# Kernel tuning notes

Measured on AMD Instinct MI355X. Metric: run time of the kernel, lower is better.

The kernel has to match this reference:

```python
import jax, jax.numpy as jnp
import numpy as np

H = 32  # hidden size

def _lstm_layer(x, Wih, Whh, bih, bhh):
    # x: [B, T, in]; Wih: [4H, in]; Whh: [4H, H]; biases: [4H]
    # Precompute input contribution for all timesteps (one big GEMM).
    xg = jnp.einsum('bti,gi->btg', x, Wih) + (bih + bhh)  # [B, T, 4H]
    B = x.shape[0]
    h0 = jnp.zeros((B, H), x.dtype)
    c0 = jnp.zeros((B, H), x.dtype)

    def step(carry, xt):
        h, c = carry
        g = xt + h @ Whh.T                      # [B, 4H]
        i, f, gg, o = jnp.split(g, 4, axis=-1)   # PyTorch gate order: i,f,g,o
        i = jax.nn.sigmoid(i)
        f = jax.nn.sigmoid(f)
        gg = jnp.tanh(gg)
        o = jax.nn.sigmoid(o)
        c = f * c + i * gg
        h = o * jnp.tanh(c)
        return (h, c), h

    (_, _), hs = jax.lax.scan(step, (h0, c0), jnp.swapaxes(xg, 0, 1))  # hs: [T, B, H]
    return jnp.swapaxes(hs, 0, 1)  # [B, T, H]


def setup_inputs() -> dict:
    key = jax.random.key(0)
    ks = jax.random.split(key, 11)
    B, T = 4096, 1024
    s = 1.0 / np.sqrt(H)  # PyTorch LSTM init scale
    f32 = jnp.float32
    return {
        'x':    jax.random.normal(ks[0], (B, T, 1), dtype=f32),
        'Wih0': jax.random.uniform(ks[1], (4 * H, 1), dtype=f32, minval=-s, maxval=s),
        'Whh0': jax.random.uniform(ks[2], (4 * H, H), dtype=f32, minval=-s, maxval=s),
        'bih0': jax.random.uniform(ks[3], (4 * H,), dtype=f32, minval=-s, maxval=s),
        'bhh0': jax.random.uniform(ks[4], (4 * H,), dtype=f32, minval=-s, maxval=s),
        'Wih1': jax.random.uniform(ks[5], (4 * H, H), dtype=f32, minval=-s, maxval=s),
        'Whh1': jax.random.uniform(ks[6], (4 * H, H), dtype=f32, minval=-s, maxval=s),
        'bih1': jax.random.uniform(ks[7], (4 * H,), dtype=f32, minval=-s, maxval=s),
        'bhh1': jax.random.uniform(ks[8], (4 * H,), dtype=f32, minval=-s, maxval=s),
        'Wfc':  jax.random.uniform(ks[9], (1, H), dtype=f32, minval=-s, maxval=s),
        'bfc':  jax.random.uniform(ks[10], (1,), dtype=f32, minval=-s, maxval=s),
    }


def reference(x, Wih0, Whh0, bih0, bhh0, Wih1, Whh1, bih1, bhh1, Wfc, bfc):
    h1 = _lstm_layer(x, Wih0, Whh0, bih0, bhh0)   # [B, T, H]
    h2 = _lstm_layer(h1, Wih1, Whh1, bih1, bhh1)  # [B, T, H]
    last = h2[:, -1, :]                            # [B, H]
    return last @ Wfc.T + bfc                      # [B, 1]
```

## Files before the change

### kernel.cpp

```cpp
#include <hip/hip_runtime.h>

#define HSZ  32
#define TLEN 1024
#define PS   40

typedef _Float16 half8 __attribute__((ext_vector_type(8)));
typedef float    f32x4 __attribute__((ext_vector_type(4)));

__device__ __forceinline__ float rcp_f(float x){ return __builtin_amdgcn_rcpf(x); }
__device__ __forceinline__ float exp2_f(float x){ return __builtin_amdgcn_exp2f(x); }
#define SCL_S (-1.442695040888963f)
#define SCL_T ( 2.885390081777927f)

__device__ __forceinline__ f32x4 mfma16(half8 a, half8 b, f32x4 c){
  return __builtin_amdgcn_mfma_f32_16x16x32_f16(a, b, c, 0, 0, 0);
}
__device__ __forceinline__ void lds_barrier(){
  asm volatile("s_waitcnt lgkmcnt(0)\n\ts_barrier" ::: "memory");
}

#define ACT4(A0,A1,A2,A3, CV, IV, FV, GV, OV)                  \
  { float Zi_ = exp2_f(A0), Zf_ = exp2_f(A1);                  \
    float Zg_ = exp2_f(A2), Zo_ = exp2_f(A3);                  \
    float di_ = 1.f+Zi_, df_ = 1.f+Zf_;                        \
    float dg_ = 1.f+Zg_, dq_ = 1.f+Zo_;                        \
    float r1_ = rcp_f(di_*df_); IV = r1_*df_; FV = r1_*di_;    \
    float r2_ = rcp_f(dg_*dq_);                                \
    GV = fmaf(-2.f, r2_*dq_, 1.f); OV = r2_*dg_;               \
    CV = fmaf(FV, CV, IV*GV); }

#define TANHPAIR(CA, CB, OA, OB, HA, HB)                       \
  { float ZA_ = exp2_f(SCL_T*(CA)), ZB_ = exp2_f(SCL_T*(CB));  \
    float dA_ = 1.f+ZA_, dB_ = 1.f+ZB_;                        \
    float re_ = rcp_f(dA_*dB_);                                \
    float qA_ = re_*dB_*(OA), qB_ = re_*dA_*(OB);              \
    HA = fmaf(-2.f, qA_, OA); HB = fmaf(-2.f, qB_, OB); }

__global__ __launch_bounds__(512, 2) void lstm2_pc(
    const float* __restrict__ x,
    const float* __restrict__ Wih0, const float* __restrict__ Whh0,
    const float* __restrict__ bih0, const float* __restrict__ bhh0,
    const float* __restrict__ Wih1, const float* __restrict__ Whh1,
    const float* __restrict__ bih1, const float* __restrict__ bhh1,
    const float* __restrict__ Wfc,  const float* __restrict__ bfc,
    float* __restrict__ out, int Tn)
{
  __shared__ __align__(16) _Float16 hpl[2][2][16*PS];

  const int tid = threadIdx.x;
  const int w   = tid >> 6;
  const int l   = tid & 63;
  const int col = l & 15;
  const int g   = l >> 4;
  const int wl  = w & 3;
  const int b0  = blockIdx.x * 16;
  const bool isL0 = (w < 4);

  const int rdI = col*PS + 8*g;
  const int wrA = col*PS + 8*wl + g;
  const int wrB = wrA + 4;
  const float sA = ((col & 3) == 2) ? SCL_T : SCL_S;
  const float scj[4] = {SCL_S, SCL_S, SCL_T, SCL_S};
  const f32x4 zero4 = {0.f, 0.f, 0.f, 0.f};

  for (int i = tid; i < 2*2*16*PS; i += 512) (&hpl[0][0][0])[i] = (_Float16)0.0f;

  float wxA[4], wxB[4], bsA[4], bsB[4];
  #pragma unroll
  for (int j = 0; j < 4; ++j){
    int rA = 32*j + 8*wl + g, rB = rA + 4;
    wxA[j] = Wih0[rA] * scj[j];
    wxB[j] = Wih0[rB] * scj[j];
    bsA[j] = (bih0[rA] + bhh0[rA]) * scj[j];
    bsB[j] = (bih1 == bih1 ? (bih0[rB] + bhh0[rB]) : 0.f) * scj[j];
  }
  const float* xp = x + (size_t)(b0 + col) * Tn;

  __syncthreads();

  if (isL0){
    float x0 = xp[0];
    float c0A = 0.f, c0B = 0.f, iA,fA,gA,oA, iB,fB,gB,oB, h0A, h0B;
    ACT4(fmaf(x0,wxA[0],bsA[0]), fmaf(x0,wxA[1],bsA[1]),
         fmaf(x0,wxA[2],bsA[2]), fmaf(x0,wxA[3],bsA[3]), c0A, iA,fA,gA,oA);
    ACT4(fmaf(x0,wxB[0],bsB[0]), fmaf(x0,wxB[1],bsB[1]),
         fmaf(x0,wxB[2],bsB[2]), fmaf(x0,wxB[3],bsB[3]), c0B, iB,fB,gB,oB);
    TANHPAIR(c0A, c0B, oA, oB, h0A, h0B);
    hpl[0][0][wrA] = (_Float16)h0A;
    hpl[0][0][wrB] = (_Float16)h0B;
    wxA[0] = wxA[0];
    ;
  }
  __syncthreads();

  float h1Av = 0.f, h1Bv = 0.f;

  if (isL0){
    const int prowA = 32*(col & 3) + 8*wl + (col >> 2);
    half8 WhA, WlA, WhB, WlB;
    {
      const float* pA = Whh0 + prowA*HSZ + 8*g;
      const float* pB = pA + 4*HSZ;
      #pragma unroll
      for (int j = 0; j < 8; ++j){
        float vA = pA[j]*sA, vB = pB[j]*sA;
        _Float16 a = (_Float16)vA; WhA[j] = a; WlA[j] = (_Float16)(vA - (float)a);
        _Float16 b = (_Float16)vB; WhB[j] = b; WlB[j] = (_Float16)(vB - (float)b);
      }
    }
    float c0A = 0.f, c0B = 0.f;
    {
      float x0 = xp[0];
      float iA,fA,gA,oA, iB,fB,gB,oB;
      ACT4(fmaf(x0,wxA[0],bsA[0]), fmaf(x0,wxA[1],bsA[1]),
           fmaf(x0,wxA[2],bsA[2]), fmaf(x0,wxA[3],bsA[3]), c0A, iA,fA,gA,oA);
      ACT4(fmaf(x0,wxB[0],bsB[0]), fmaf(x0,wxB[1],bsB[1]),
           fmaf(x0,wxB[2],bsB[2]), fmaf(x0,wxB[3],bsB[3]), c0B, iB,fB,gB,oB);
    }
    half8 Bh0 = *(const half8*)&hpl[0][0][rdI];
    float xv = xp[1];

#define L0STEP(Q, XNI)                                                     \
    {                                                                      \
      float xn = xp[(XNI)];                                                \
      f32x4 eA, eB;                                                        \
      eA[0]=fmaf(xv,wxA[0],bsA[0]); eA[1]=fmaf(xv,wxA[1],bsA[1]);          \
      eA[2]=fmaf(xv,wxA[2],bsA[2]); eA[3]=fmaf(xv,wxA[3],bsA[3]);          \
      eB[0]=fmaf(xv,wxB[0],bsB[0]); eB[1]=fmaf(xv,wxB[1],bsB[1]);          \
      eB[2]=fmaf(xv,wxB[2],bsB[2]); eB[3]=fmaf(xv,wxB[3],bsB[3]);          \
      __builtin_amdgcn_s_setprio(1);                                       \
      eA = mfma16(WhA, Bh0, eA);  eB = mfma16(WhB, Bh0, eB);               \
      eA = mfma16(WlA, Bh0, eA);  eB = mfma16(WlB, Bh0, eB);               \
      __builtin_amdgcn_s_setprio(0);                                       \
      float iA,fA,gA,oA, iB,fB,gB,oB, h0A, h0B;                            \
      ACT4(eA[0],eA[1],eA[2],eA[3], c0A, iA,fA,gA,oA);                     \
      ACT4(eB[0],eB[1],eB[2],eB[3], c0B, iB,fB,gB,oB);                     \
      TANHPAIR(c0A, c0B, oA, oB, h0A, h0B);                                \
      hpl[(Q)][0][wrA] = (_Float16)h0A;                                    \
      hpl[(Q)][0][wrB] = (_Float16)h0B;                                    \
      lds_barrier();                                                       \
      Bh0 = *(const half8*)&hpl[(Q)][0][rdI];                              \
      xv = xn;                                                             \
    }

    for (int T0 = 0; T0 < Tn; T0 += 2){
      L0STEP(1, (T0+2 < Tn) ? T0+2 : Tn-1);
      L0STEP(0, (T0+3 < Tn) ? T0+3 : Tn-1);
    }
#undef L0STEP
  } else {
    const int prowA = 32*(col & 3) + 8*wl + (col >> 2);
    half8 WIhA, WIlA, WIhB, WIlB, WHhA, WHlA, WHhB, WHlB;
    {
      const float* iA_ = Wih1 + prowA*HSZ + 8*g;
      const float* iB_ = iA_ + 4*HSZ;
      const float* hA_ = Whh1 + prowA*HSZ + 8*g;
      const float* hB_ = hA_ + 4*HSZ;
      #pragma unroll
      for (int j = 0; j < 8; ++j){
        float v0 = iA_[j]*sA, v1 = iB_[j]*sA, v2 = hA_[j]*sA, v3 = hB_[j]*sA;
        _Float16 a = (_Float16)v0; WIhA[j] = a; WIlA[j] = (_Float16)(v0 - (float)a);
        _Float16 b = (_Float16)v1; WIhB[j] = b; WIlB[j] = (_Float16)(v1 - (float)b);
        _Float16 c = (_Float16)v2; WHhA[j] = c; WHlA[j] = (_Float16)(v2 - (float)c);
        _Float16 d = (_Float16)v3; WHhB[j] = d; WHlB[j] = (_Float16)(v3 - (float)d);
      }
    }
    f32x4 bias1A, bias1B;
    #pragma unroll
    for (int j = 0; j < 4; ++j){
      int rA = 32*j + 8*wl + g, rB = rA + 4;
      bias1A[j] = (bih1[rA] + bhh1[rA]) * scj[j];
      bias1B[j] = (bih1[rB] + bhh1[rB]) * scj[j];
    }
    float c1A = 0.f, c1B = 0.f;
    half8 Bh0 = *(const half8*)&hpl[0][0][rdI];
    half8 Bh1 = *(const half8*)&hpl[0][1][rdI];

#define L1STEP(Q)                                                          \
    {                                                                      \
      f32x4 uA, uB, vvA, vvB;                                              \
      __builtin_amdgcn_s_setprio(1);                                       \
      uA  = mfma16(WHhA, Bh1, bias1A);  uB  = mfma16(WHhB, Bh1, bias1B);   \
      vvA = mfma16(WIhA, Bh0, zero4);   vvB = mfma16(WIhB, Bh0, zero4);    \
      uA  = mfma16(WHlA, Bh1, uA);      uB  = mfma16(WHlB, Bh1, uB);       \
      vvA = mfma16(WIlA, Bh0, vvA);     vvB = mfma16(WIlB, Bh0, vvB);      \
      __builtin_amdgcn_s_setprio(0);                                       \
      f32x4 aA = uA + vvA, aB = uB + vvB;                                  \
      float iA,fA,gA,oA, iB,fB,gB,oB;                                      \
      ACT4(aA[0],aA[1],aA[2],aA[3], c1A, iA,fA,gA,oA);                     \
      ACT4(aB[0],aB[1],aB[2],aB[3], c1B, iB,fB,gB,oB);                     \
      TANHPAIR(c1A, c1B, oA, oB, h1Av, h1Bv);                              \
      hpl[(Q)][1][wrA] = (_Float16)h1Av;                                   \
      hpl[(Q)][1][wrB] = (_Float16)h1Bv;                                   \
      lds_barrier();                                                       \
      Bh0 = *(const half8*)&hpl[(Q)][0][rdI];                              \
      Bh1 = *(const half8*)&hpl[(Q)][1][rdI];                              \
    }

    for (int T0 = 0; T0 < Tn; T0 += 2){
      L1STEP(1);
      L1STEP(0);
    }
#undef L1STEP
  }

  __syncthreads();
  float* sc = (float*)&hpl[0][0][0];
  if (w >= 4){
    sc[(8*wl + g)*17 + col]     = h1Av;
    sc[(8*wl + 4 + g)*17 + col] = h1Bv;
  }
  __syncthreads();
  if (tid < 16){
    float acc = bfc[0];
    #pragma unroll 8
    for (int k = 0; k < HSZ; ++k) acc = fmaf(sc[k*17 + tid], Wfc[k], acc);
    out[b0 + tid] = acc;
  }
}

extern "C" void kernel_launch(void* const* d_in, const int* in_sizes, int n_in,
                              void* d_out, int out_size, void* d_ws, size_t ws_size,
                              hipStream_t stream) {
  const float* x    = (const float*)d_in[0];
  const float* Wih0 = (const float*)d_in[1];
  const float* Whh0 = (const float*)d_in[2];
  const float* bih0 = (const float*)d_in[3];
  const float* bhh0 = (const float*)d_in[4];
  const float* Wih1 = (const float*)d_in[5];
  const float* Whh1 = (const float*)d_in[6];
  const float* bih1 = (const float*)d_in[7];
  const float* bhh1 = (const float*)d_in[8];
  const float* Wfc  = (const float*)d_in[9];
  const float* bfc  = (const float*)d_in[10];
  float* out = (float*)d_out;

  const int Tn = TLEN;
  const int B  = in_sizes[0] / Tn;

  dim3 block(512);
  dim3 grid(B / 16);
  hipLaunchKernelGGL(lstm2_pc, grid, block, 0, stream,
                     x, Wih0, Whh0, bih0, bhh0, Wih1, Whh1, bih1, bhh1,
                     Wfc, bfc, out, Tn);
}
```

Measured before the change: 411.8 us.

## Split LSTM gate work across 16 waves per block instead of 8

The block grows from 8 to 16 waves: 8 waves for layer 0 and 8 for layer 1. Each wave now handles one 16-row slice of the gate matrix instead of two, which halves the MFMA and activation work per wave on the serial per-timestep critical path. The cost is more waves meeting at every per-step barrier and higher occupancy demands, with launch bounds raised to 1024 threads and 4 blocks per CU. Whether the per-step latency actually drops depends on barrier overhead versus the shortened dependency chain.

```diff
diff --git a/kernel.cpp b/kernel.cpp
--- a/kernel.cpp
+++ b/kernel.cpp
@@ -29,14 +29,12 @@
     GV = fmaf(-2.f, r2_*dq_, 1.f); OV = r2_*dg_;               \
     CV = fmaf(FV, CV, IV*GV); }
 
-#define TANHPAIR(CA, CB, OA, OB, HA, HB)                       \
-  { float ZA_ = exp2_f(SCL_T*(CA)), ZB_ = exp2_f(SCL_T*(CB));  \
-    float dA_ = 1.f+ZA_, dB_ = 1.f+ZB_;                        \
-    float re_ = rcp_f(dA_*dB_);                                \
-    float qA_ = re_*dB_*(OA), qB_ = re_*dA_*(OB);              \
-    HA = fmaf(-2.f, qA_, OA); HB = fmaf(-2.f, qB_, OB); }
-
-__global__ __launch_bounds__(512, 2) void lstm2_pc(
+#define HOUT(CV, OV, HV)                                       \
+  { float Zc_ = exp2_f(SCL_T*(CV));                            \
+    float rc_ = rcp_f(1.f + Zc_);                              \
+    HV = fmaf(-2.f, rc_*(OV), OV); }
+
+__global__ __launch_bounds__(1024, 4) void lstm2_w16(
     const float* __restrict__ x,
     const float* __restrict__ Wih0, const float* __restrict__ Whh0,
     const float* __restrict__ bih0, const float* __restrict__ bhh0,
@@ -52,92 +50,89 @@
   const int l   = tid & 63;
   const int col = l & 15;
   const int g   = l >> 4;
-  const int wl  = w & 3;
   const int b0  = blockIdx.x * 16;
-  const bool isL0 = (w < 4);
+  const bool isL0 = (w < 8);
+  const int wl  = isL0 ? w : (w - 8);
+  const int st  = 4*wl + g;
 
   const int rdI = col*PS + 8*g;
-  const int wrA = col*PS + 8*wl + g;
-  const int wrB = wrA + 4;
+  const int wrI = col*PS + st;
   const float sA = ((col & 3) == 2) ? SCL_T : SCL_S;
   const float scj[4] = {SCL_S, SCL_S, SCL_T, SCL_S};
   const f32x4 zero4 = {0.f, 0.f, 0.f, 0.f};
-
-  for (int i = tid; i < 2*2*16*PS; i += 512) (&hpl[0][0][0])[i] = (_Float16)0.0f;
-
-  float wxA[4], wxB[4], bsA[4], bsB[4];
-  #pragma unroll
-  for (int j = 0; j < 4; ++j){
-    int rA = 32*j + 8*wl + g, rB = rA + 4;
-    wxA[j] = Wih0[rA] * scj[j];
-    wxB[j] = Wih0[rB] * scj[j];
-    bsA[j] = (bih0[rA] + bhh0[rA]) * scj[j];
-    bsB[j] = (bih1 == bih1 ? (bih0[rB] + bhh0[rB]) : 0.f) * scj[j];
-  }
+  const int prow = 32*(col & 3) + 4*wl + (col >> 2);
+
+  for (int i = tid; i < 2*2*16*PS; i += 1024) (&hpl[0][0][0])[i] = (_Float16)0.0f;
+
+  half8 WAh, WAl, WBh, WBl;
+  f32x4 bias1;
+  float wx[4], bs0[4];
+  half8 WIh, WIl;
   const float* xp = x + (size_t)(b0 + col) * Tn;
+
+  if (isL0){
+    const float* p0 = Whh0 + prow*HSZ + 8*g;
+    #pragma unroll
+    for (int j = 0; j < 8; ++j){
+      float v0 = p0[j]*sA;
+      _Float16 a = (_Float16)v0; WAh[j] = a; WAl[j] = (_Float16)(v0 - (float)a);
+    }
+    #pragma unroll
+    for (int j = 0; j < 4; ++j){
+      int r  = 32*j + st;
+      wx[j]  = Wih0[r] * scj[j];
+      bs0[j] = (bih0[r] + bhh0[r]) * scj[j];
+    }
+  } else {
+    const float* pH = Whh1 + prow*HSZ + 8*g;
+    const float* pI = Wih1 + prow*HSZ + 8*g;
+    #pragma unroll
+    for (int j = 0; j < 8; ++j){
+      float v2 = pH[j]*sA, v1 = pI[j]*sA;
+      _Float16 c = (_Float16)v2; WAh[j] = c; WAl[j] = (_Float16)(v2 - (float)c);
+      _Float16 b = (_Float16)v1; WIh[j] = b; WIl[j] = (_Float16)(v1 - (float)b);
+    }
+    #pragma unroll
+    for (int j = 0; j < 4; ++j){
+      int r = 32*j + st;
+      bias1[j] = (bih1[r] + bhh1[r]) * scj[j];
+    }
+  }
+  (void)WBh; (void)WBl;
+
+  float cSt = 0.f, hFin = 0.f;
 
   __syncthreads();
 
   if (isL0){
     float x0 = xp[0];
-    float c0A = 0.f, c0B = 0.f, iA,fA,gA,oA, iB,fB,gB,oB, h0A, h0B;
-    ACT4(fmaf(x0,wxA[0],bsA[0]), fmaf(x0,wxA[1],bsA[1]),
-         fmaf(x0,wxA[2],bsA[2]), fmaf(x0,wxA[3],bsA[3]), c0A, iA,fA,gA,oA);
-    ACT4(fmaf(x0,wxB[0],bsB[0]), fmaf(x0,wxB[1],bsB[1]),
-         fmaf(x0,wxB[2],bsB[2]), fmaf(x0,wxB[3],bsB[3]), c0B, iB,fB,gB,oB);
-    TANHPAIR(c0A, c0B, oA, oB, h0A, h0B);
-    hpl[0][0][wrA] = (_Float16)h0A;
-    hpl[0][0][wrB] = (_Float16)h0B;
-    wxA[0] = wxA[0];
-    ;
-  }
-  __syncthreads();
-
-  float h1Av = 0.f, h1Bv = 0.f;
+    float iv, fv, gv, ov;
+    ACT4(fmaf(x0,wx[0],bs0[0]), fmaf(x0,wx[1],bs0[1]),
+         fmaf(x0,wx[2],bs0[2]), fmaf(x0,wx[3],bs0[3]), cSt, iv,fv,gv,ov);
+    float h0;
+    HOUT(cSt, ov, h0);
+    hpl[0][0][wrI] = (_Float16)h0;
+  }
+  __syncthreads();
 
   if (isL0){
-    const int prowA = 32*(col & 3) + 8*wl + (col >> 2);
-    half8 WhA, WlA, WhB, WlB;
-    {
-      const float* pA = Whh0 + prowA*HSZ + 8*g;
-      const float* pB = pA + 4*HSZ;
-      #pragma unroll
-      for (int j = 0; j < 8; ++j){
-        float vA = pA[j]*sA, vB = pB[j]*sA;
-        _Float16 a = (_Float16)vA; WhA[j] = a; WlA[j] = (_Float16)(vA - (float)a);
-        _Float16 b = (_Float16)vB; WhB[j] = b; WlB[j] = (_Float16)(vB - (float)b);
-      }
-    }
-    float c0A = 0.f, c0B = 0.f;
-    {
-      float x0 = xp[0];
-      float iA,fA,gA,oA, iB,fB,gB,oB;
-      ACT4(fmaf(x0,wxA[0],bsA[0]), fmaf(x0,wxA[1],bsA[1]),
-           fmaf(x0,wxA[2],bsA[2]), fmaf(x0,wxA[3],bsA[3]), c0A, iA,fA,gA,oA);
-      ACT4(fmaf(x0,wxB[0],bsB[0]), fmaf(x0,wxB[1],bsB[1]),
-           fmaf(x0,wxB[2],bsB[2]), fmaf(x0,wxB[3],bsB[3]), c0B, iB,fB,gB,oB);
-    }
     half8 Bh0 = *(const half8*)&hpl[0][0][rdI];
     float xv = xp[1];
 
 #define L0STEP(Q, XNI)                                                     \
     {                                                                      \
       float xn = xp[(XNI)];                                                \
-      f32x4 eA, eB;                                                        \
-      eA[0]=fmaf(xv,wxA[0],bsA[0]); eA[1]=fmaf(xv,wxA[1],bsA[1]);          \
-      eA[2]=fmaf(xv,wxA[2],bsA[2]); eA[3]=fmaf(xv,wxA[3],bsA[3]);          \
-      eB[0]=fmaf(xv,wxB[0],bsB[0]); eB[1]=fmaf(xv,wxB[1],bsB[1]);          \
-      eB[2]=fmaf(xv,wxB[2],bsB[2]); eB[3]=fmaf(xv,wxB[3],bsB[3]);          \
+      f32x4 e;                                                             \
+      e[0]=fmaf(xv,wx[0],bs0[0]); e[1]=fmaf(xv,wx[1],bs0[1]);              \
+      e[2]=fmaf(xv,wx[2],bs0[2]); e[3]=fmaf(xv,wx[3],bs0[3]);              \
       __builtin_amdgcn_s_setprio(1);                                       \
-      eA = mfma16(WhA, Bh0, eA);  eB = mfma16(WhB, Bh0, eB);               \
-      eA = mfma16(WlA, Bh0, eA);  eB = mfma16(WlB, Bh0, eB);               \
+      e = mfma16(WAh, Bh0, e);                                             \
+      e = mfma16(WAl, Bh0, e);                                             \
       __builtin_amdgcn_s_setprio(0);                                       \
-      float iA,fA,gA,oA, iB,fB,gB,oB, h0A, h0B;                            \
-      ACT4(eA[0],eA[1],eA[2],eA[3], c0A, iA,fA,gA,oA);                     \
-      ACT4(eB[0],eB[1],eB[2],eB[3], c0B, iB,fB,gB,oB);                     \
-      TANHPAIR(c0A, c0B, oA, oB, h0A, h0B);                                \
-      hpl[(Q)][0][wrA] = (_Float16)h0A;                                    \
-      hpl[(Q)][0][wrB] = (_Float16)h0B;                                    \
+      float iv, fv, gv, ov, h0;                                            \
+      ACT4(e[0],e[1],e[2],e[3], cSt, iv,fv,gv,ov);                         \
+      HOUT(cSt, ov, h0);                                                   \
+      hpl[(Q)][0][wrI] = (_Float16)h0;                                     \
       lds_barrier();                                                       \
       Bh0 = *(const half8*)&hpl[(Q)][0][rdI];                              \
       xv = xn;                                                             \
@@ -149,49 +144,23 @@
     }
 #undef L0STEP
   } else {
-    const int prowA = 32*(col & 3) + 8*wl + (col >> 2);
-    half8 WIhA, WIlA, WIhB, WIlB, WHhA, WHlA, WHhB, WHlB;
-    {
-      const float* iA_ = Wih1 + prowA*HSZ + 8*g;
-      const float* iB_ = iA_ + 4*HSZ;
-      const float* hA_ = Whh1 + prowA*HSZ + 8*g;
-      const float* hB_ = hA_ + 4*HSZ;
-      #pragma unroll
-      for (int j = 0; j < 8; ++j){
-        float v0 = iA_[j]*sA, v1 = iB_[j]*sA, v2 = hA_[j]*sA, v3 = hB_[j]*sA;
-        _Float16 a = (_Float16)v0; WIhA[j] = a; WIlA[j] = (_Float16)(v0 - (float)a);
-        _Float16 b = (_Float16)v1; WIhB[j] = b; WIlB[j] = (_Float16)(v1 - (float)b);
-        _Float16 c = (_Float16)v2; WHhA[j] = c; WHlA[j] = (_Float16)(v2 - (float)c);
-        _Float16 d = (_Float16)v3; WHhB[j] = d; WHlB[j] = (_Float16)(v3 - (float)d);
-      }
-    }
-    f32x4 bias1A, bias1B;
-    #pragma unroll
-    for (int j = 0; j < 4; ++j){
-      int rA = 32*j + 8*wl + g, rB = rA + 4;
-      bias1A[j] = (bih1[rA] + bhh1[rA]) * scj[j];
-      bias1B[j] = (bih1[rB] + bhh1[rB]) * scj[j];
-    }
-    float c1A = 0.f, c1B = 0.f;
     half8 Bh0 = *(const half8*)&hpl[0][0][rdI];
     half8 Bh1 = *(const half8*)&hpl[0][1][rdI];
 
 #define L1STEP(Q)                                                          \
     {                                                                      \
-      f32x4 uA, uB, vvA, vvB;                                              \
+      f32x4 u, vv;                                                         \
       __builtin_amdgcn_s_setprio(1);                                       \
-      uA  = mfma16(WHhA, Bh1, bias1A);  uB  = mfma16(WHhB, Bh1, bias1B);   \
-      vvA = mfma16(WIhA, Bh0, zero4);   vvB = mfma16(WIhB, Bh0, zero4);    \
-      uA  = mfma16(WHlA, Bh1, uA);      uB  = mfma16(WHlB, Bh1, uB);       \
-      vvA = mfma16(WIlA, Bh0, vvA);     vvB = mfma16(WIlB, Bh0, vvB);      \
+      u  = mfma16(WAh, Bh1, bias1);                                        \
+      vv = mfma16(WIh, Bh0, zero4);                                        \
+      u  = mfma16(WAl, Bh1, u);                                            \
+      vv = mfma16(WIl, Bh0, vv);                                           \
       __builtin_amdgcn_s_setprio(0);                                       \
-      f32x4 aA = uA + vvA, aB = uB + vvB;                                  \
-      float iA,fA,gA,oA, iB,fB,gB,oB;                                      \
-      ACT4(aA[0],aA[1],aA[2],aA[3], c1A, iA,fA,gA,oA);                     \
-      ACT4(aB[0],aB[1],aB[2],aB[3], c1B, iB,fB,gB,oB);                     \
-      TANHPAIR(c1A, c1B, oA, oB, h1Av, h1Bv);                              \
-      hpl[(Q)][1][wrA] = (_Float16)h1Av;                                   \
-      hpl[(Q)][1][wrB] = (_Float16)h1Bv;                                   \
+      f32x4 a = u + vv;                                                    \
+      float iv, fv, gv, ov;                                                \
+      ACT4(a[0],a[1],a[2],a[3], cSt, iv,fv,gv,ov);                         \
+      HOUT(cSt, ov, hFin);                                                 \
+      hpl[(Q)][1][wrI] = (_Float16)hFin;                                   \
       lds_barrier();                                                       \
       Bh0 = *(const half8*)&hpl[(Q)][0][rdI];                              \
       Bh1 = *(const half8*)&hpl[(Q)][1][rdI];                              \
@@ -206,9 +175,8 @@
 
   __syncthreads();
   float* sc = (float*)&hpl[0][0][0];
-  if (w >= 4){
-    sc[(8*wl + g)*17 + col]     = h1Av;
-    sc[(8*wl + 4 + g)*17 + col] = h1Bv;
+  if (!isL0){
+    sc[st*17 + col] = hFin;
   }
   __syncthreads();
   if (tid < 16){
@@ -238,9 +206,9 @@
   const int Tn = TLEN;
   const int B  = in_sizes[0] / Tn;
 
-  dim3 block(512);
+  dim3 block(1024);
   dim3 grid(B / 16);
-  hipLaunchKernelGGL(lstm2_pc, grid, block, 0, stream,
+  hipLaunchKernelGGL(lstm2_w16, grid, block, 0, stream,
                      x, Wih0, Whh0, bih0, bhh0, Wih1, Whh1, bih1, bhh1,
                      Wfc, bfc, out, Tn);
 }
```

Result: no change. 408.6 us (-0.8%).

## Skew layer-0 and layer-1 phases with two barriers per step

Applied to the files above, without the earlier changes.

Restructures the per-timestep schedule so layer-0 waves run their MFMA for the next step right after publishing h0, while layer-1 waves do their MFMAs and then their activations in a separate barrier phase. Each step now has two barriers, so layer-0 and layer-1 activation work sit in different phases and overlap with the other layer's matrix work instead of both hitting the same critical path. Layer-1 now keeps a single h1 buffer and reads h0 from a double buffer, and the setprio hints are dropped. The price is an extra barrier per timestep, and the two layers depend on a careful phase alignment for correctness.

```diff
diff --git a/kernel.cpp b/kernel.cpp
--- a/kernel.cpp
+++ b/kernel.cpp
@@ -19,15 +19,16 @@
   asm volatile("s_waitcnt lgkmcnt(0)\n\ts_barrier" ::: "memory");
 }
 
-#define ACT4(A0,A1,A2,A3, CV, IV, FV, GV, OV)                  \
+#define ACT4(A0,A1,A2,A3, CV, OV)                              \
   { float Zi_ = exp2_f(A0), Zf_ = exp2_f(A1);                  \
     float Zg_ = exp2_f(A2), Zo_ = exp2_f(A3);                  \
     float di_ = 1.f+Zi_, df_ = 1.f+Zf_;                        \
     float dg_ = 1.f+Zg_, dq_ = 1.f+Zo_;                        \
-    float r1_ = rcp_f(di_*df_); IV = r1_*df_; FV = r1_*di_;    \
+    float r1_ = rcp_f(di_*df_);                                \
+    float IV_ = r1_*df_, FV_ = r1_*di_;                        \
     float r2_ = rcp_f(dg_*dq_);                                \
-    GV = fmaf(-2.f, r2_*dq_, 1.f); OV = r2_*dg_;               \
-    CV = fmaf(FV, CV, IV*GV); }
+    float GV_ = fmaf(-2.f, r2_*dq_, 1.f); OV = r2_*dg_;        \
+    CV = fmaf(FV_, CV, IV_*GV_); }
 
 #define TANHPAIR(CA, CB, OA, OB, HA, HB)                       \
   { float ZA_ = exp2_f(SCL_T*(CA)), ZB_ = exp2_f(SCL_T*(CB));  \
@@ -36,7 +37,7 @@
     float qA_ = re_*dB_*(OA), qB_ = re_*dA_*(OB);              \
     HA = fmaf(-2.f, qA_, OA); HB = fmaf(-2.f, qB_, OB); }
 
-__global__ __launch_bounds__(512, 2) void lstm2_pc(
+__global__ __launch_bounds__(512, 2) void lstm2_skew(
     const float* __restrict__ x,
     const float* __restrict__ Wih0, const float* __restrict__ Whh0,
     const float* __restrict__ bih0, const float* __restrict__ bhh0,
@@ -45,16 +46,18 @@
     const float* __restrict__ Wfc,  const float* __restrict__ bfc,
     float* __restrict__ out, int Tn)
 {
-  __shared__ __align__(16) _Float16 hpl[2][2][16*PS];
+  __shared__ __align__(16) _Float16 H0[2][16*PS];
+  __shared__ __align__(16) _Float16 H1[16*PS];
+  __shared__ float sc[32*17];
 
   const int tid = threadIdx.x;
   const int w   = tid >> 6;
   const int l   = tid & 63;
   const int col = l & 15;
   const int g   = l >> 4;
-  const int wl  = w & 3;
   const int b0  = blockIdx.x * 16;
   const bool isL0 = (w < 4);
+  const int wl  = isL0 ? w : (w - 4);
 
   const int rdI = col*PS + 8*g;
   const int wrA = col*PS + 8*wl + g;
@@ -62,151 +65,150 @@
   const float sA = ((col & 3) == 2) ? SCL_T : SCL_S;
   const float scj[4] = {SCL_S, SCL_S, SCL_T, SCL_S};
   const f32x4 zero4 = {0.f, 0.f, 0.f, 0.f};
-
-  for (int i = tid; i < 2*2*16*PS; i += 512) (&hpl[0][0][0])[i] = (_Float16)0.0f;
-
+  const int prowA = 32*(col & 3) + 8*wl + (col >> 2);
+
+  for (int i = tid; i < (2*16 + 16)*PS; i += 512) (&H0[0][0])[i] = (_Float16)0.0f;
+
+  const float* xp = x + (size_t)(b0 + col) * Tn;
+  const int Tm1 = Tn - 1;
+
+  half8 WhA, WlA, WhB, WlB;
+  half8 WIhA, WIlA, WIhB, WIlB;
   float wxA[4], wxB[4], bsA[4], bsB[4];
-  #pragma unroll
-  for (int j = 0; j < 4; ++j){
-    int rA = 32*j + 8*wl + g, rB = rA + 4;
-    wxA[j] = Wih0[rA] * scj[j];
-    wxB[j] = Wih0[rB] * scj[j];
-    bsA[j] = (bih0[rA] + bhh0[rA]) * scj[j];
-    bsB[j] = (bih1 == bih1 ? (bih0[rB] + bhh0[rB]) : 0.f) * scj[j];
-  }
-  const float* xp = x + (size_t)(b0 + col) * Tn;
-
-  __syncthreads();
+  f32x4 bias1A, bias1B;
 
   if (isL0){
-    float x0 = xp[0];
-    float c0A = 0.f, c0B = 0.f, iA,fA,gA,oA, iB,fB,gB,oB, h0A, h0B;
-    ACT4(fmaf(x0,wxA[0],bsA[0]), fmaf(x0,wxA[1],bsA[1]),
-         fmaf(x0,wxA[2],bsA[2]), fmaf(x0,wxA[3],bsA[3]), c0A, iA,fA,gA,oA);
-    ACT4(fmaf(x0,wxB[0],bsB[0]), fmaf(x0,wxB[1],bsB[1]),
-         fmaf(x0,wxB[2],bsB[2]), fmaf(x0,wxB[3],bsB[3]), c0B, iB,fB,gB,oB);
-    TANHPAIR(c0A, c0B, oA, oB, h0A, h0B);
-    hpl[0][0][wrA] = (_Float16)h0A;
-    hpl[0][0][wrB] = (_Float16)h0B;
-    wxA[0] = wxA[0];
-    ;
-  }
-  __syncthreads();
-
-  float h1Av = 0.f, h1Bv = 0.f;
-
-  if (isL0){
-    const int prowA = 32*(col & 3) + 8*wl + (col >> 2);
-    half8 WhA, WlA, WhB, WlB;
-    {
-      const float* pA = Whh0 + prowA*HSZ + 8*g;
-      const float* pB = pA + 4*HSZ;
-      #pragma unroll
-      for (int j = 0; j < 8; ++j){
-        float vA = pA[j]*sA, vB = pB[j]*sA;
-        _Float16 a = (_Float16)vA; WhA[j] = a; WlA[j] = (_Float16)(vA - (float)a);
-        _Float16 b = (_Float16)vB; WhB[j] = b; WlB[j] = (_Float16)(vB - (float)b);
-      }
-    }
-    float c0A = 0.f, c0B = 0.f;
-    {
-      float x0 = xp[0];
-      float iA,fA,gA,oA, iB,fB,gB,oB;
-      ACT4(fmaf(x0,wxA[0],bsA[0]), fmaf(x0,wxA[1],bsA[1]),
-           fmaf(x0,wxA[2],bsA[2]), fmaf(x0,wxA[3],bsA[3]), c0A, iA,fA,gA,oA);
-      ACT4(fmaf(x0,wxB[0],bsB[0]), fmaf(x0,wxB[1],bsB[1]),
-           fmaf(x0,wxB[2],bsB[2]), fmaf(x0,wxB[3],bsB[3]), c0B, iB,fB,gB,oB);
-    }
-    half8 Bh0 = *(const half8*)&hpl[0][0][rdI];
-    float xv = xp[1];
-
-#define L0STEP(Q, XNI)                                                     \
-    {                                                                      \
-      float xn = xp[(XNI)];                                                \
-      f32x4 eA, eB;                                                        \
-      eA[0]=fmaf(xv,wxA[0],bsA[0]); eA[1]=fmaf(xv,wxA[1],bsA[1]);          \
-      eA[2]=fmaf(xv,wxA[2],bsA[2]); eA[3]=fmaf(xv,wxA[3],bsA[3]);          \
-      eB[0]=fmaf(xv,wxB[0],bsB[0]); eB[1]=fmaf(xv,wxB[1],bsB[1]);          \
-      eB[2]=fmaf(xv,wxB[2],bsB[2]); eB[3]=fmaf(xv,wxB[3],bsB[3]);          \
-      __builtin_amdgcn_s_setprio(1);                                       \
-      eA = mfma16(WhA, Bh0, eA);  eB = mfma16(WhB, Bh0, eB);               \
-      eA = mfma16(WlA, Bh0, eA);  eB = mfma16(WlB, Bh0, eB);               \
-      __builtin_amdgcn_s_setprio(0);                                       \
-      float iA,fA,gA,oA, iB,fB,gB,oB, h0A, h0B;                            \
-      ACT4(eA[0],eA[1],eA[2],eA[3], c0A, iA,fA,gA,oA);                     \
-      ACT4(eB[0],eB[1],eB[2],eB[3], c0B, iB,fB,gB,oB);                     \
-      TANHPAIR(c0A, c0B, oA, oB, h0A, h0B);                                \
-      hpl[(Q)][0][wrA] = (_Float16)h0A;                                    \
-      hpl[(Q)][0][wrB] = (_Float16)h0B;                                    \
-      lds_barrier();                                                       \
-      Bh0 = *(const half8*)&hpl[(Q)][0][rdI];                              \
-      xv = xn;                                                             \
-    }
-
-    for (int T0 = 0; T0 < Tn; T0 += 2){
-      L0STEP(1, (T0+2 < Tn) ? T0+2 : Tn-1);
-      L0STEP(0, (T0+3 < Tn) ? T0+3 : Tn-1);
-    }
-#undef L0STEP
+    const float* pA = Whh0 + prowA*HSZ + 8*g;
+    const float* pB = pA + 4*HSZ;
+    #pragma unroll
+    for (int j = 0; j < 8; ++j){
+      float vA = pA[j]*sA, vB = pB[j]*sA;
+      _Float16 a = (_Float16)vA; WhA[j] = a; WlA[j] = (_Float16)(vA - (float)a);
+      _Float16 b = (_Float16)vB; WhB[j] = b; WlB[j] = (_Float16)(vB - (float)b);
+    }
+    #pragma unroll
+    for (int j = 0; j < 4; ++j){
+      int rA = 32*j + 8*wl + g, rB = rA + 4;
+      wxA[j] = Wih0[rA] * scj[j];
+      wxB[j] = Wih0[rB] * scj[j];
+      bsA[j] = (bih0[rA] + bhh0[rA]) * scj[j];
+      bsB[j] = (bih0[rB] + bhh0[rB]) * scj[j];
+    }
   } else {
-    const int prowA = 32*(col & 3) + 8*wl + (col >> 2);
-    half8 WIhA, WIlA, WIhB, WIlB, WHhA, WHlA, WHhB, WHlB;
-    {
-      const float* iA_ = Wih1 + prowA*HSZ + 8*g;
-      const float* iB_ = iA_ + 4*HSZ;
-      const float* hA_ = Whh1 + prowA*HSZ + 8*g;
-      const float* hB_ = hA_ + 4*HSZ;
-      #pragma unroll
-      for (int j = 0; j < 8; ++j){
-        float v0 = iA_[j]*sA, v1 = iB_[j]*sA, v2 = hA_[j]*sA, v3 = hB_[j]*sA;
-        _Float16 a = (_Float16)v0; WIhA[j] = a; WIlA[j] = (_Float16)(v0 - (float)a);
-        _Float16 b = (_Float16)v1; WIhB[j] = b; WIlB[j] = (_Float16)(v1 - (float)b);
-        _Float16 c = (_Float16)v2; WHhA[j] = c; WHlA[j] = (_Float16)(v2 - (float)c);
-        _Float16 d = (_Float16)v3; WHhB[j] = d; WHlB[j] = (_Float16)(v3 - (float)d);
-      }
-    }
-    f32x4 bias1A, bias1B;
+    const float* hA_ = Whh1 + prowA*HSZ + 8*g;
+    const float* hB_ = hA_ + 4*HSZ;
+    const float* iA_ = Wih1 + prowA*HSZ + 8*g;
+    const float* iB_ = iA_ + 4*HSZ;
+    #pragma unroll
+    for (int j = 0; j < 8; ++j){
+      float v0 = hA_[j]*sA, v1 = hB_[j]*sA, v2 = iA_[j]*sA, v3 = iB_[j]*sA;
+      _Float16 a = (_Float16)v0; WhA[j]  = a; WlA[j]  = (_Float16)(v0 - (float)a);
+      _Float16 b = (_Float16)v1; WhB[j]  = b; WlB[j]  = (_Float16)(v1 - (float)b);
+      _Float16 c = (_Float16)v2; WIhA[j] = c; WIlA[j] = (_Float16)(v2 - (float)c);
+      _Float16 d = (_Float16)v3; WIhB[j] = d; WIlB[j] = (_Float16)(v3 - (float)d);
+    }
     #pragma unroll
     for (int j = 0; j < 4; ++j){
       int rA = 32*j + 8*wl + g, rB = rA + 4;
       bias1A[j] = (bih1[rA] + bhh1[rA]) * scj[j];
       bias1B[j] = (bih1[rB] + bhh1[rB]) * scj[j];
     }
-    float c1A = 0.f, c1B = 0.f;
-    half8 Bh0 = *(const half8*)&hpl[0][0][rdI];
-    half8 Bh1 = *(const half8*)&hpl[0][1][rdI];
-
-#define L1STEP(Q)                                                          \
+  }
+
+  float c0A = 0.f, c0B = 0.f;
+  float c1A = 0.f, c1B = 0.f;
+  float h1Av = 0.f, h1Bv = 0.f;
+
+  __syncthreads();
+
+  if (isL0){
+    float x0 = xp[0];
+    float oA_, oB_, h0A, h0B;
+    ACT4(fmaf(x0,wxA[0],bsA[0]), fmaf(x0,wxA[1],bsA[1]),
+         fmaf(x0,wxA[2],bsA[2]), fmaf(x0,wxA[3],bsA[3]), c0A, oA_);
+    ACT4(fmaf(x0,wxB[0],bsB[0]), fmaf(x0,wxB[1],bsB[1]),
+         fmaf(x0,wxB[2],bsB[2]), fmaf(x0,wxB[3],bsB[3]), c0B, oB_);
+    TANHPAIR(c0A, c0B, oA_, oB_, h0A, h0B);
+    H0[0][wrA] = (_Float16)h0A;
+    H0[0][wrB] = (_Float16)h0B;
+  }
+  __syncthreads();
+
+  if (isL0){
+    half8 Bh0 = *(const half8*)&H0[0][rdI];
+    f32x4 eA, eB;
+    {
+      float x1 = xp[1];
+      eA[0] = fmaf(x1, wxA[0], bsA[0]); eA[1] = fmaf(x1, wxA[1], bsA[1]);
+      eA[2] = fmaf(x1, wxA[2], bsA[2]); eA[3] = fmaf(x1, wxA[3], bsA[3]);
+      eB[0] = fmaf(x1, wxB[0], bsB[0]); eB[1] = fmaf(x1, wxB[1], bsB[1]);
+      eB[2] = fmaf(x1, wxB[2], bsB[2]); eB[3] = fmaf(x1, wxB[3], bsB[3]);
+      eA = mfma16(WhA, Bh0, eA);  eB = mfma16(WhB, Bh0, eB);
+      eA = mfma16(WlA, Bh0, eA);  eB = mfma16(WlB, Bh0, eB);
+    }
+    float xc = xp[2 <= Tm1 ? 2 : Tm1];
+
+#define L0BODY(Q, XNI)                                                     \
     {                                                                      \
-      f32x4 uA, uB, vvA, vvB;                                              \
-      __builtin_amdgcn_s_setprio(1);                                       \
-      uA  = mfma16(WHhA, Bh1, bias1A);  uB  = mfma16(WHhB, Bh1, bias1B);   \
-      vvA = mfma16(WIhA, Bh0, zero4);   vvB = mfma16(WIhB, Bh0, zero4);    \
-      uA  = mfma16(WHlA, Bh1, uA);      uB  = mfma16(WHlB, Bh1, uB);       \
-      vvA = mfma16(WIlA, Bh0, vvA);     vvB = mfma16(WIlB, Bh0, vvB);      \
-      __builtin_amdgcn_s_setprio(0);                                       \
-      f32x4 aA = uA + vvA, aB = uB + vvB;                                  \
-      float iA,fA,gA,oA, iB,fB,gB,oB;                                      \
-      ACT4(aA[0],aA[1],aA[2],aA[3], c1A, iA,fA,gA,oA);                     \
-      ACT4(aB[0],aB[1],aB[2],aB[3], c1B, iB,fB,gB,oB);                     \
-      TANHPAIR(c1A, c1B, oA, oB, h1Av, h1Bv);                              \
-      hpl[(Q)][1][wrA] = (_Float16)h1Av;                                   \
-      hpl[(Q)][1][wrB] = (_Float16)h1Bv;                                   \
-      lds_barrier();                                                       \
-      Bh0 = *(const half8*)&hpl[(Q)][0][rdI];                              \
-      Bh1 = *(const half8*)&hpl[(Q)][1][rdI];                              \
+      float xn = xp[(XNI)];                   \
+                                 \
+      float oA_, oB_, h0A, h0B;                                            \
+      ACT4(eA[0],eA[1],eA[2],eA[3], c0A, oA_);                             \
+      ACT4(eB[0],eB[1],eB[2],eB[3], c0B, oB_);                             \
+      TANHPAIR(c0A, c0B, oA_, oB_, h0A, h0B);                              \
+      H0[(Q)][wrA] = (_Float16)h0A;                                        \
+      H0[(Q)][wrB] = (_Float16)h0B;                                        \
+      lds_barrier();                                             \
+                                  \
+      Bh0 = *(const half8*)&H0[(Q)][rdI];                                  \
+      eA[0] = fmaf(xc, wxA[0], bsA[0]); eA[1] = fmaf(xc, wxA[1], bsA[1]);  \
+      eA[2] = fmaf(xc, wxA[2], bsA[2]); eA[3] = fmaf(xc, wxA[3], bsA[3]);  \
+      eB[0] = fmaf(xc, wxB[0], bsB[0]); eB[1] = fmaf(xc, wxB[1], bsB[1]);  \
+      eB[2] = fmaf(xc, wxB[2], bsB[2]); eB[3] = fmaf(xc, wxB[3], bsB[3]);  \
+      eA = mfma16(WhA, Bh0, eA);  eB = mfma16(WhB, Bh0, eB);               \
+      eA = mfma16(WlA, Bh0, eA);  eB = mfma16(WlB, Bh0, eB);               \
+      lds_barrier();                                             \
+      xc = xn;                                                             \
     }
 
     for (int T0 = 0; T0 < Tn; T0 += 2){
-      L1STEP(1);
-      L1STEP(0);
-    }
-#undef L1STEP
-  }
-
-  __syncthreads();
-  float* sc = (float*)&hpl[0][0][0];
-  if (w >= 4){
+      L0BODY(1, (T0+3 <= Tm1) ? T0+3 : Tm1);
+      L0BODY(0, (T0+4 <= Tm1) ? T0+4 : Tm1);
+    }
+#undef L0BODY
+  } else {
+#define L1BODY(R)                                                          \
+    {                                                                      \
+                                    \
+      half8 Bh0 = *(const half8*)&H0[(R)][rdI];                            \
+      half8 Bh1 = *(const half8*)&H1[rdI];                                 \
+      f32x4 uA = mfma16(WhA, Bh1, bias1A);                                 \
+      f32x4 uB = mfma16(WhB, Bh1, bias1B);                                 \
+      f32x4 vA = mfma16(WIhA, Bh0, zero4);                                 \
+      f32x4 vB = mfma16(WIhB, Bh0, zero4);                                 \
+      uA = mfma16(WlA, Bh1, uA);   uB = mfma16(WlB, Bh1, uB);              \
+      vA = mfma16(WIlA, Bh0, vA);  vB = mfma16(WIlB, Bh0, vB);             \
+      lds_barrier();                                             \
+                                     \
+      f32x4 aA = uA + vA, aB = uB + vB;                                    \
+      float oA_, oB_;                                                      \
+      ACT4(aA[0],aA[1],aA[2],aA[3], c1A, oA_);                             \
+      ACT4(aB[0],aB[1],aB[2],aB[3], c1B, oB_);                             \
+      TANHPAIR(c1A, c1B, oA_, oB_, h1Av, h1Bv);                            \
+      H1[wrA] = (_Float16)h1Av;                                            \
+      H1[wrB] = (_Float16)h1Bv;                                            \
+      lds_barrier();                                             \
+    }
+
+    for (int T0 = 0; T0 < Tn; T0 += 2){
+      L1BODY(0);
+      L1BODY(1);
+    }
+#undef L1BODY
+  }
+
+  __syncthreads();
+  if (!isL0){
     sc[(8*wl + g)*17 + col]     = h1Av;
     sc[(8*wl + 4 + g)*17 + col] = h1Bv;
   }
@@ -240,7 +242,7 @@
 
   dim3 block(512);
   dim3 grid(B / 16);
-  hipLaunchKernelGGL(lstm2_pc, grid, block, 0, stream,
+  hipLaunchKernelGGL(lstm2_skew, grid, block, 0, stream,
                      x, Wih0, Whh0, bih0, bhh0, Wih1, Whh1, bih1, bhh1,
                      Wfc, bfc, out, Tn);
 }
```

New measurement: 454.1 us. 10.3% more time.
